# Optimization experiments

Measured on AMD Instinct MI355X. Metric: run time of the kernel, lower is better.

Reference implementation:

```python
import jax, jax.numpy as jnp
import numpy as np

H = 16  # attention heads


def setup_inputs() -> dict:
    key = jax.random.key(0)
    k0, k1, k2 = jax.random.split(key, 3)
    B, T, C = 2, 2048, 1024
    x = jax.random.normal(k0, (B, T, C), dtype=jnp.float32)
    W_attn = jax.random.normal(k1, (3 * C, C), dtype=jnp.float32) * 0.02
    W_proj = jax.random.normal(k2, (C, C), dtype=jnp.float32) * 0.02
    b_proj = jnp.zeros((C,), dtype=jnp.float32)
    return {"x": x, "W_attn": W_attn, "W_proj": W_proj, "b_proj": b_proj}


def reference(x, W_attn, W_proj, b_proj):
    # Eval-mode (dropout = identity), rotational_embeddings=False, flash=False path.
    B, T, C = x.shape
    d = C // H
    qkv = jnp.einsum('btc,fc->btf', x, W_attn)          # [B,T,3C] fused QKV proj
    q, k, v = jnp.split(qkv, 3, axis=-1)
    # [B,T,C] -> [B,H,T,d]
    q = q.reshape(B, T, H, d).transpose(0, 2, 1, 3)
    k = k.reshape(B, T, H, d).transpose(0, 2, 1, 3)
    v = v.reshape(B, T, H, d).transpose(0, 2, 1, 3)
    scale = 1.0 / np.sqrt(d).astype(np.float32)
    att = jnp.einsum('bhqd,bhkd->bhqk', q, k) * scale    # full TxT scores (no mask)
    att = jax.nn.softmax(att, axis=-1)
    y = jnp.einsum('bhqk,bhkd->bhqd', att, v)            # [B,H,T,d]
    y = y.transpose(0, 2, 1, 3).reshape(B, T, C)
    return jnp.einsum('btc,oc->bto', y, W_proj) + b_proj
```

## Files before the change

kernel.cpp:

```cpp
#include <hip/hip_runtime.h>
#include <hip/hip_bf16.h>
#include <stdint.h>

typedef __attribute__((ext_vector_type(8))) short bf16x8;
typedef __attribute__((ext_vector_type(4))) float f32x4;
typedef __attribute__((ext_vector_type(4))) unsigned u32x4;

#define MFMA16(A,B,C) __builtin_amdgcn_mfma_f32_16x16x32_bf16(A,B,C,0,0,0)


__device__ inline void gld_lds16(const __hip_bfloat16* g, __hip_bfloat16* l) {
  __builtin_amdgcn_global_load_lds(
      (const __attribute__((address_space(1))) void*)g,
      (__attribute__((address_space(3))) void*)l, 16, 0, 0);
}

__device__ inline void cvt_store8(const float* __restrict__ g,
                                  __hip_bfloat16* __restrict__ l) {
  float4 u0 = *(const float4*)g;
  float4 u1 = *(const float4*)(g + 4);
  __hip_bfloat162 t[4];
  t[0] = __float22bfloat162_rn(float2{u0.x, u0.y});
  t[1] = __float22bfloat162_rn(float2{u0.z, u0.w});
  t[2] = __float22bfloat162_rn(float2{u1.x, u1.y});
  t[3] = __float22bfloat162_rn(float2{u1.z, u1.w});
  *(int4*)l = *(const int4*)t;
}

__device__ inline void comb_store8(const __hip_bfloat16* __restrict__ a,
                                   const __hip_bfloat16* __restrict__ b,
                                   float rinv,
                                   __hip_bfloat16* __restrict__ l) {
  int4 av = *(const int4*)a;
  int4 bv = *(const int4*)b;
  const __hip_bfloat162* ap = (const __hip_bfloat162*)&av;
  const __hip_bfloat162* bp = (const __hip_bfloat162*)&bv;
  __hip_bfloat162 t[4];
#pragma unroll
  for (int i = 0; i < 4; i++) {
    float2 fa = __bfloat1622float2(ap[i]);
    float2 fb = __bfloat1622float2(bp[i]);
    t[i] = __float22bfloat162_rn(float2{(fa.x + fb.x) * rinv,
                                        (fa.y + fb.y) * rinv});
  }
  *(int4*)l = *(const int4*)t;
}

__device__ inline unsigned pkbf(float a, float b) {
  __hip_bfloat162 t = __float22bfloat162_rn(float2{a, b});
  return *(unsigned*)&t;
}

__device__ inline void quad_mix(unsigned &a, unsigned &b) {
#if __has_builtin(__builtin_amdgcn_permlane32_swap) && __has_builtin(__builtin_amdgcn_permlane16_swap)
  auto r1 = __builtin_amdgcn_permlane32_swap(a, b, false, false);
  auto r2 = __builtin_amdgcn_permlane16_swap(r1[0], r1[1], false, false);
  a = r2[0];
  b = r2[1];
#else
  int lane = (int)(threadIdx.x & 63);
  int g = lane >> 4;
  int lm = lane & 15;
  int slo = (((g << 1) & 3) << 4) | lm;
  int shi = ((((g << 1) | 1) & 3) << 4) | lm;
  unsigned t0 = (unsigned)__shfl((int)a, slo, 64);
  unsigned t1 = (unsigned)__shfl((int)b, slo, 64);
  unsigned t2 = (unsigned)__shfl((int)a, shi, 64);
  unsigned t3 = (unsigned)__shfl((int)b, shi, 64);
  bool hi = g >= 2;
  unsigned na = hi ? t1 : t0;
  unsigned nb = hi ? t3 : t2;
  a = na;
  b = nb;
#endif
}

__global__ __launch_bounds__(256)
void gemm_qkv(const float* __restrict__ A,
              const float* __restrict__ B,
              __hip_bfloat16* __restrict__ C,
              __hip_bfloat16* __restrict__ vtg,
              int M, int N, int K)
{
  __shared__ __align__(16) __hip_bfloat16 As[128 * 32];
  __shared__ __align__(16) __hip_bfloat16 Bs[128 * 32];

  const int tid  = threadIdx.x;
  const int lane = tid & 63;
  const int w    = tid >> 6;
  const int lm   = lane & 15;
  const int g    = lane >> 4;

  const int bm = blockIdx.y * 128;
  const int bn = blockIdx.x * 128;
  const int rm = (w >> 1) * 64;
  const int cn = (w & 1) * 64;

  const int row0 = tid >> 2;
  const int kc   = (tid & 3) * 8;

  const f32x4 fzero = {0.0f, 0.0f, 0.0f, 0.0f};
  f32x4 acc[4][4];
  for (int i = 0; i < 4; i++)
    for (int j = 0; j < 4; j++)
      acc[i][j] = fzero;

  for (int k0 = 0; k0 < K; k0 += 32) {
    __syncthreads();
#pragma unroll
    for (int p = 0; p < 2; p++) {
      int row = row0 + 64 * p;
      cvt_store8(A + (size_t)(bm + row) * K + k0 + kc, &As[row * 32 + kc]);
      cvt_store8(B + (size_t)(bn + row) * K + k0 + kc, &Bs[row * 32 + kc]);
    }
    __syncthreads();

    bf16x8 af[4], bfr[4];
#pragma unroll
    for (int i = 0; i < 4; i++)
      af[i] = *(const bf16x8*)&As[(rm + 16 * i + lm) * 32 + 8 * g];
#pragma unroll
    for (int j = 0; j < 4; j++)
      bfr[j] = *(const bf16x8*)&Bs[(cn + 16 * j + lm) * 32 + 8 * g];
#pragma unroll
    for (int i = 0; i < 4; i++)
#pragma unroll
      for (int j = 0; j < 4; j++)
        acc[i][j] = MFMA16(af[i], bfr[j], acc[i][j]);
  }

  if (bn >= 2048) {
#pragma unroll
    for (int j = 0; j < 4; j++) {
      int colv = bn + cn + 16 * j + lm - 2048;
      int vh = colv >> 6, dd = colv & 63;
#pragma unroll
      for (int i = 0; i < 4; i++) {
        int m0 = bm + rm + 16 * i + 4 * g;
        int bb = m0 >> 11, t0 = m0 & 2047;
        __hip_bfloat16 t4[4];
#pragma unroll
        for (int r = 0; r < 4; r++) t4[r] = __float2bfloat16(acc[i][j][r]);
        *(int2*)&vtg[((size_t)(bb * 16 + vh) * 64 + dd) * 2048 + t0] =
            *(const int2*)t4;
      }
    }
    return;
  }

  const float qs = (bn < 1024) ? (0.125f * 1.4426950408889634f) : 1.0f;
#pragma unroll
  for (int j = 0; j < 4; j++) {
    int coln = bn + cn + 16 * j + lm;
#pragma unroll
    for (int i = 0; i < 4; i++) {
#pragma unroll
      for (int r = 0; r < 4; r++) {
        int rowm = bm + rm + 16 * i + 4 * g + r;
        C[(size_t)rowm * N + coln] = __float2bfloat16(acc[i][j][r] * qs);
      }
    }
  }
}

__global__ __launch_bounds__(256)
void gemm_out(const __hip_bfloat16* __restrict__ po,
              const float* __restrict__ pl,
              const float* __restrict__ Bw,
              const float* __restrict__ bias,
              float* __restrict__ out,
              int M, int N, int K)
{
  __shared__ __align__(16) __hip_bfloat16 As[128 * 32];
  __shared__ __align__(16) __hip_bfloat16 Bs[128 * 32];

  const int tid  = threadIdx.x;
  const int lane = tid & 63;
  const int w    = tid >> 6;
  const int lm   = lane & 15;
  const int g    = lane >> 4;

  const int bm = blockIdx.y * 128;
  const int bn = blockIdx.x * 128;
  const int rm = (w >> 1) * 64;
  const int cn = (w & 1) * 64;

  const int row0 = tid >> 2;
  const int kc   = (tid & 3) * 8;

  const f32x4 fzero = {0.0f, 0.0f, 0.0f, 0.0f};
  f32x4 acc[4][4];
  for (int i = 0; i < 4; i++)
    for (int j = 0; j < 4; j++)
      acc[i][j] = fzero;

  for (int k0 = 0; k0 < K; k0 += 32) {
    const int h = (k0 + kc) >> 6;
    __syncthreads();
#pragma unroll
    for (int p = 0; p < 2; p++) {
      int row = row0 + 64 * p;
      int m = bm + row;
      float la = pl[m * 16 + h];
      float lb = pl[4096 * 16 + m * 16 + h];
      float rinv = 1.0f / (la + lb);
      comb_store8(po + (size_t)m * 1024 + k0 + kc,
                  po + (size_t)4096 * 1024 + (size_t)m * 1024 + k0 + kc,
                  rinv, &As[row * 32 + kc]);
      cvt_store8(Bw + (size_t)(bn + row) * K + k0 + kc, &Bs[row * 32 + kc]);
    }
    __syncthreads();

    bf16x8 af[4], bfr[4];
#pragma unroll
    for (int i = 0; i < 4; i++)
      af[i] = *(const bf16x8*)&As[(rm + 16 * i + lm) * 32 + 8 * g];
#pragma unroll
    for (int j = 0; j < 4; j++)
      bfr[j] = *(const bf16x8*)&Bs[(cn + 16 * j + lm) * 32 + 8 * g];
#pragma unroll
    for (int i = 0; i < 4; i++)
#pragma unroll
      for (int j = 0; j < 4; j++)
        acc[i][j] = MFMA16(af[i], bfr[j], acc[i][j]);
  }

#pragma unroll
  for (int j = 0; j < 4; j++) {
    int coln = bn + cn + 16 * j + lm;
    float bv = bias[coln];
#pragma unroll
    for (int i = 0; i < 4; i++) {
#pragma unroll
      for (int r = 0; r < 4; r++) {
        int rowm = bm + rm + 16 * i + 4 * g + r;
        out[(size_t)rowm * N + coln] = acc[i][j][r] + bv;
      }
    }
  }
}

__global__ __launch_bounds__(256)
void mha(const __hip_bfloat16* __restrict__ qkv,
         const __hip_bfloat16* __restrict__ vtg,
         __hip_bfloat16* __restrict__ po,
         float* __restrict__ pl,
         int nsteps)
{
  const int T = 2048, F = 3072, Cc = 1024;
  const int bh = blockIdx.x;
  const int b  = bh >> 4, h = bh & 15;
  const int qb0 = blockIdx.y * 128;
  const int z   = blockIdx.z;
  const int kvb = z * 32 * nsteps;

  const int tid  = threadIdx.x;
  const int lane = tid & 63;
  const int w    = tid >> 6;
  const int lm   = lane & 15;
  const int g    = lane >> 4;

  __shared__ __align__(16) __hip_bfloat16 Ks[2][32 * 64];
  __shared__ __align__(16) __hip_bfloat16 Vs[2][64 * 32];

  const size_t rowbase = (size_t)b * T * F;
  const int hoff = h * 64;
  const __hip_bfloat16* Kbase = qkv + rowbase + 1024 + hoff;
  const __hip_bfloat16* Vtb   = vtg + (size_t)(b * 16 + h) * 64 * 2048;

  const int qw = qb0 + 32 * w;
  bf16x8 aq[2][2];
#pragma unroll
  for (int mt = 0; mt < 2; mt++)
#pragma unroll
    for (int e = 0; e < 2; e++)
      aq[mt][e] = *(const bf16x8*)
          &qkv[rowbase + (size_t)(qw + 16 * mt + lm) * F + hoff + 32 * e + 8 * g];

  const f32x4 fzero = {0.0f, 0.0f, 0.0f, 0.0f};
  f32x4 yacc[2][4];
  float lsum[2] = {0.0f, 0.0f};
#pragma unroll
  for (int mt = 0; mt < 2; mt++)
#pragma unroll
    for (int c = 0; c < 4; c++) yacc[mt][c] = fzero;

  const int r0  = tid >> 3;
  const int swK = (tid & 7) ^ (r0 & 7);
  const int vdd = tid >> 2;
  const int vk  = (tid & 3) ^ ((tid >> 3) & 3);
  const int sxK = lm & 7;
  const int sxV = (lm >> 1) & 3;

  gld_lds16(Kbase + (size_t)(kvb + r0) * F + swK * 8, &Ks[0][tid * 8]);
  gld_lds16(Vtb + (size_t)vdd * 2048 + kvb + vk * 8, &Vs[0][tid * 8]);

  for (int t = 0; t < nsteps; t++) {
    const int buf = t & 1;
    __syncthreads();
    if (t + 1 < nsteps) {
      const int kvn = kvb + (t + 1) * 32;
      gld_lds16(Kbase + (size_t)(kvn + r0) * F + swK * 8, &Ks[buf ^ 1][tid * 8]);
      gld_lds16(Vtb + (size_t)vdd * 2048 + kvn + vk * 8, &Vs[buf ^ 1][tid * 8]);
    }

    bf16x8 kf[2][2];
#pragma unroll
    for (int c2 = 0; c2 < 2; c2++) {
      kf[c2][0] = *(const bf16x8*)&Ks[buf][(16 * c2 + lm) * 64 + ((0 + g) ^ sxK) * 8];
      kf[c2][1] = *(const bf16x8*)&Ks[buf][(16 * c2 + lm) * 64 + ((4 + g) ^ sxK) * 8];
    }
#pragma unroll
    for (int mt = 0; mt < 2; mt++) {
      f32x4 st[2];
#pragma unroll
      for (int c2 = 0; c2 < 2; c2++) {
        st[c2] = MFMA16(kf[c2][0], aq[mt][0], fzero);
        st[c2] = MFMA16(kf[c2][1], aq[mt][1], st[c2]);
      }

      unsigned pkv[2][2];
#pragma unroll
      for (int c2 = 0; c2 < 2; c2++)
#pragma unroll
        for (int u = 0; u < 2; u++) {
          float p0 = __builtin_amdgcn_exp2f(st[c2][2 * u]);
          float p1 = __builtin_amdgcn_exp2f(st[c2][2 * u + 1]);
          lsum[mt] += p0 + p1;
          pkv[c2][u] = pkbf(p0, p1);
        }

      unsigned f0 = pkv[0][0], f2 = pkv[1][0];
      quad_mix(f0, f2);
      unsigned f1 = pkv[0][1], f3 = pkv[1][1];
      quad_mix(f1, f3);
      u32x4 fv = {f0, f1, f2, f3};
      bf16x8 ap = __builtin_bit_cast(bf16x8, fv);

#pragma unroll
      for (int c = 0; c < 4; c++) {
        bf16x8 bv = *(const bf16x8*)&Vs[buf][(16 * c + lm) * 32 + (g ^ sxV) * 8];
        yacc[mt][c] = MFMA16(ap, bv, yacc[mt][c]);
      }
    }
  }

  float lred[2];
#pragma unroll
  for (int mt = 0; mt < 2; mt++) {
    float ls = lsum[mt];
    ls += __shfl_xor(ls, 16);
    ls += __shfl_xor(ls, 32);
    lred[mt] = ls;
  }

  __hip_bfloat16* pz = po + (size_t)z * 4096 * 1024;
  float* plz = pl + (size_t)z * 4096 * 16;
#pragma unroll
  for (int mt = 0; mt < 2; mt++) {
#pragma unroll
    for (int c = 0; c < 4; c++)
#pragma unroll
      for (int r = 0; r < 4; r++) {
        int qrow = qw + 16 * mt + 4 * g + r;
        pz[(size_t)(b * T + qrow) * Cc + hoff + 16 * c + lm] =
            __float2bfloat16(yacc[mt][c][r]);
      }
    if (lane < 16)
      plz[(b * T + qw + 16 * mt + lane) * 16 + h] = lred[mt];
  }
}

extern "C" void kernel_launch(void* const* d_in, const int* in_sizes, int n_in,
                              void* d_out, int out_size, void* d_ws, size_t ws_size,
                              hipStream_t stream)
{
  const float* x  = (const float*)d_in[0];
  const float* Wa = (const float*)d_in[1];
  const float* Wp = (const float*)d_in[2];
  const float* bp = (const float*)d_in[3];
  float* out = (float*)d_out;

  const int BT = 4096, C = 1024, F3 = 3072;
  char* ws = (char*)d_ws;
  __hip_bfloat16* qkv  = (__hip_bfloat16*)ws;
  __hip_bfloat16* vtg  = (__hip_bfloat16*)(ws + 25165824);
  __hip_bfloat16* Opar = (__hip_bfloat16*)(ws + 33554432);
  float*          lpar = (float*)(ws + 50331648);

  gemm_qkv<<<dim3(F3 / 128, BT / 128), 256, 0, stream>>>(x, Wa, qkv, vtg,
                                                         BT, F3, C);
  mha<<<dim3(32, 16, 2), 256, 0, stream>>>(qkv, vtg, Opar, lpar, 32);
  gemm_out<<<dim3(C / 128, BT / 128), 256, 0, stream>>>(Opar, lpar, Wp, bp, out,
                                                        BT, C, C);
}
```

Measured before the change: 223.5 us.

## Register-prefetch next K tile in both GEMMs and halve gemm_out N tile

Both GEMM kernels now load the next K-slice from global memory into registers before the MFMA work on the current tile, so global-load latency overlaps with compute; the barrier is moved to the end of each iteration. gemm_out also switches from 128x128 to 128x64 tiles, doubling its grid from 256 to 512 blocks so more CUs are kept busy. The costs are higher register pressure from the prefetch buffers and more redundant A-tile loads in gemm_out.

```diff
diff --git a/kernel.cpp b/kernel.cpp
--- a/kernel.cpp
+++ b/kernel.cpp
@@ -15,10 +15,8 @@
       (__attribute__((address_space(3))) void*)l, 16, 0, 0);
 }
 
-__device__ inline void cvt_store8(const float* __restrict__ g,
-                                  __hip_bfloat16* __restrict__ l) {
-  float4 u0 = *(const float4*)g;
-  float4 u1 = *(const float4*)(g + 4);
+__device__ inline void cvt_store8r(float4 u0, float4 u1,
+                                   __hip_bfloat16* __restrict__ l) {
   __hip_bfloat162 t[4];
   t[0] = __float22bfloat162_rn(float2{u0.x, u0.y});
   t[1] = __float22bfloat162_rn(float2{u0.z, u0.w});
@@ -27,12 +25,8 @@
   *(int4*)l = *(const int4*)t;
 }
 
-__device__ inline void comb_store8(const __hip_bfloat16* __restrict__ a,
-                                   const __hip_bfloat16* __restrict__ b,
-                                   float rinv,
-                                   __hip_bfloat16* __restrict__ l) {
-  int4 av = *(const int4*)a;
-  int4 bv = *(const int4*)b;
+__device__ inline void comb_store8r(int4 av, int4 bv, float rinv,
+                                    __hip_bfloat16* __restrict__ l) {
   const __hip_bfloat162* ap = (const __hip_bfloat162*)&av;
   const __hip_bfloat162* bp = (const __hip_bfloat162*)&bv;
   __hip_bfloat162 t[4];
@@ -99,21 +93,35 @@
   const int row0 = tid >> 2;
   const int kc   = (tid & 3) * 8;
 
+  float4 pa[2][2], pb[2][2];
+  auto ldtile = [&](int k0) {
+#pragma unroll
+    for (int p = 0; p < 2; p++) {
+      const float* ga = A + (size_t)(bm + row0 + 64 * p) * K + k0 + kc;
+      pa[p][0] = *(const float4*)ga;
+      pa[p][1] = *(const float4*)(ga + 4);
+      const float* gb = B + (size_t)(bn + row0 + 64 * p) * K + k0 + kc;
+      pb[p][0] = *(const float4*)gb;
+      pb[p][1] = *(const float4*)(gb + 4);
+    }
+  };
+
   const f32x4 fzero = {0.0f, 0.0f, 0.0f, 0.0f};
   f32x4 acc[4][4];
   for (int i = 0; i < 4; i++)
     for (int j = 0; j < 4; j++)
       acc[i][j] = fzero;
 
+  ldtile(0);
   for (int k0 = 0; k0 < K; k0 += 32) {
-    __syncthreads();
 #pragma unroll
     for (int p = 0; p < 2; p++) {
       int row = row0 + 64 * p;
-      cvt_store8(A + (size_t)(bm + row) * K + k0 + kc, &As[row * 32 + kc]);
-      cvt_store8(B + (size_t)(bn + row) * K + k0 + kc, &Bs[row * 32 + kc]);
+      cvt_store8r(pa[p][0], pa[p][1], &As[row * 32 + kc]);
+      cvt_store8r(pb[p][0], pb[p][1], &Bs[row * 32 + kc]);
     }
     __syncthreads();
+    if (k0 + 32 < K) ldtile(k0 + 32);
 
     bf16x8 af[4], bfr[4];
 #pragma unroll
@@ -127,6 +135,7 @@
 #pragma unroll
       for (int j = 0; j < 4; j++)
         acc[i][j] = MFMA16(af[i], bfr[j], acc[i][j]);
+    __syncthreads();
   }
 
   if (bn >= 2048) {
@@ -172,7 +181,7 @@
               int M, int N, int K)
 {
   __shared__ __align__(16) __hip_bfloat16 As[128 * 32];
-  __shared__ __align__(16) __hip_bfloat16 Bs[128 * 32];
+  __shared__ __align__(16) __hip_bfloat16 Bs[64 * 32];
 
   const int tid  = threadIdx.x;
   const int lane = tid & 63;
@@ -181,52 +190,64 @@
   const int g    = lane >> 4;
 
   const int bm = blockIdx.y * 128;
-  const int bn = blockIdx.x * 128;
+  const int bn = blockIdx.x * 64;
   const int rm = (w >> 1) * 64;
-  const int cn = (w & 1) * 64;
+  const int cn = (w & 1) * 32;
 
   const int row0 = tid >> 2;
   const int kc   = (tid & 3) * 8;
 
+  int4  qa[2], qb[2];
+  float la[2], lb[2];
+  float4 wb0, wb1;
+  auto ldtile = [&](int k0) {
+    const int h = k0 >> 6;
+#pragma unroll
+    for (int p = 0; p < 2; p++) {
+      int m = bm + row0 + 64 * p;
+      qa[p] = *(const int4*)(po + (size_t)m * 1024 + k0 + kc);
+      qb[p] = *(const int4*)(po + (size_t)4096 * 1024 + (size_t)m * 1024 + k0 + kc);
+      la[p] = pl[m * 16 + h];
+      lb[p] = pl[4096 * 16 + m * 16 + h];
+    }
+    const float* gb = Bw + (size_t)(bn + row0) * K + k0 + kc;
+    wb0 = *(const float4*)gb;
+    wb1 = *(const float4*)(gb + 4);
+  };
+
   const f32x4 fzero = {0.0f, 0.0f, 0.0f, 0.0f};
-  f32x4 acc[4][4];
+  f32x4 acc[4][2];
   for (int i = 0; i < 4; i++)
-    for (int j = 0; j < 4; j++)
+    for (int j = 0; j < 2; j++)
       acc[i][j] = fzero;
 
+  ldtile(0);
   for (int k0 = 0; k0 < K; k0 += 32) {
-    const int h = (k0 + kc) >> 6;
+#pragma unroll
+    for (int p = 0; p < 2; p++)
+      comb_store8r(qa[p], qb[p], 1.0f / (la[p] + lb[p]),
+                   &As[(row0 + 64 * p) * 32 + kc]);
+    cvt_store8r(wb0, wb1, &Bs[row0 * 32 + kc]);
     __syncthreads();
-#pragma unroll
-    for (int p = 0; p < 2; p++) {
-      int row = row0 + 64 * p;
-      int m = bm + row;
-      float la = pl[m * 16 + h];
-      float lb = pl[4096 * 16 + m * 16 + h];
-      float rinv = 1.0f / (la + lb);
-      comb_store8(po + (size_t)m * 1024 + k0 + kc,
-                  po + (size_t)4096 * 1024 + (size_t)m * 1024 + k0 + kc,
-                  rinv, &As[row * 32 + kc]);
-      cvt_store8(Bw + (size_t)(bn + row) * K + k0 + kc, &Bs[row * 32 + kc]);
-    }
-    __syncthreads();
-
-    bf16x8 af[4], bfr[4];
+    if (k0 + 32 < K) ldtile(k0 + 32);
+
+    bf16x8 af[4], bfr[2];
 #pragma unroll
     for (int i = 0; i < 4; i++)
       af[i] = *(const bf16x8*)&As[(rm + 16 * i + lm) * 32 + 8 * g];
 #pragma unroll
-    for (int j = 0; j < 4; j++)
+    for (int j = 0; j < 2; j++)
       bfr[j] = *(const bf16x8*)&Bs[(cn + 16 * j + lm) * 32 + 8 * g];
 #pragma unroll
     for (int i = 0; i < 4; i++)
 #pragma unroll
-      for (int j = 0; j < 4; j++)
+      for (int j = 0; j < 2; j++)
         acc[i][j] = MFMA16(af[i], bfr[j], acc[i][j]);
-  }
-
-#pragma unroll
-  for (int j = 0; j < 4; j++) {
+    __syncthreads();
+  }
+
+#pragma unroll
+  for (int j = 0; j < 2; j++) {
     int coln = bn + cn + 16 * j + lm;
     float bv = bias[coln];
 #pragma unroll
@@ -391,6 +412,6 @@
   gemm_qkv<<<dim3(F3 / 128, BT / 128), 256, 0, stream>>>(x, Wa, qkv, vtg,
                                                          BT, F3, C);
   mha<<<dim3(32, 16, 2), 256, 0, stream>>>(qkv, vtg, Opar, lpar, 32);
-  gemm_out<<<dim3(C / 128, BT / 128), 256, 0, stream>>>(Opar, lpar, Wp, bp, out,
-                                                        BT, C, C);
-}
+  gemm_out<<<dim3(C / 64, BT / 128), 256, 0, stream>>>(Opar, lpar, Wp, bp, out,
+                                                       BT, C, C);
+}
```

New measurement: 209.2 us. 6.4% less time.
